# Performance work log

Measured on AMD Instinct MI355X. Metric: run time of the kernel, lower is better.

Reference implementation:

```python
import jax, jax.numpy as jnp
import numpy as np

L, B, T, C, H, D, F, W = 2, 2, 2048, 1024, 16, 64, 4096, 256
NEG = -1e9
EPS = 1e-6


def _rms(x, g):
    return x * jax.lax.rsqrt(jnp.mean(x * x, axis=-1, keepdims=True) + EPS) * g


def setup_inputs() -> dict:
    key = jax.random.key(0)
    ks = jax.random.split(key, 12)
    s = 0.02
    return {
        "x": jax.random.normal(ks[0], (B, T, C), jnp.float32),
        "retrieval_context": jax.random.normal(ks[1], (B, C), jnp.float32),
        "norm1_g": jnp.ones((L, C), jnp.float32),
        "Wqkv": jax.random.normal(ks[2], (L, C, 3 * C), jnp.float32) * s,
        "Wproj": jax.random.normal(ks[3], (L, C, C), jnp.float32) * s,
        "gate_W": jax.random.normal(ks[4], (L, C, 3), jnp.float32) * 0.01,
        "gate_b": jnp.zeros((L, 3), jnp.float32),
        "ret_W": jax.random.normal(ks[5], (L, C, C), jnp.float32) * 0.01,
        "norm2_g": jnp.ones((L, C), jnp.float32),
        "ffn_gate_W": jax.random.normal(ks[6], (L, C, F), jnp.float32) * s,
        "ffn_up_W": jax.random.normal(ks[7], (L, C, F), jnp.float32) * s,
        "ffn_down_W": jax.random.normal(ks[8], (L, F, C), jnp.float32) * s,
    }


def reference(x, retrieval_context, norm1_g, Wqkv, Wproj, gate_W, gate_b, ret_W,
              norm2_g, ffn_gate_W, ffn_up_W, ffn_down_W):
    # Sliding-window causal mask: key j visible to query i iff i-W+1 <= j <= i
    pos = jnp.arange(T)
    allowed = (pos[None, :] <= pos[:, None]) & (pos[None, :] >= pos[:, None] - W + 1)
    mask = jnp.where(allowed, 0.0, NEG).astype(x.dtype)  # (T, T)
    scale = 1.0 / np.sqrt(D)

    for l in range(L):
        h = _rms(x, norm1_g[l])                              # (B,T,C)
        qkv = h @ Wqkv[l]                                    # (B,T,3C)
        q, k, v = jnp.split(qkv, 3, axis=-1)
        q = q.reshape(B, T, H, D).transpose(0, 2, 1, 3)       # (B,H,T,D)
        k = k.reshape(B, T, H, D).transpose(0, 2, 1, 3)
        v = v.reshape(B, T, H, D).transpose(0, 2, 1, 3)
        scores = jnp.einsum("bhqd,bhkd->bhqk", q, k) * scale + mask
        attn = jax.nn.softmax(scores, axis=-1)
        o = jnp.einsum("bhqk,bhkd->bhqd", attn, v)
        attn_out = o.transpose(0, 2, 1, 3).reshape(B, T, C) @ Wproj[l]

        # TRN disabled: trn_out == 0, gate channel 1 pinned to -1e9
        gate_logits = h @ gate_W[l] + gate_b[l]               # (B,T,3)
        gate_logits = gate_logits.at[..., 1].set(NEG)
        gates = jax.nn.softmax(gate_logits, axis=-1)

        ret_out = (retrieval_context @ ret_W[l])[:, None, :]   # (B,1,C) broadcast over T
        mixed = gates[..., 0:1] * attn_out + gates[..., 2:3] * ret_out
        x = x + mixed

        h2 = _rms(x, norm2_g[l])
        ffn = (jax.nn.silu(h2 @ ffn_gate_W[l]) * (h2 @ ffn_up_W[l])) @ ffn_down_W[l]
        x = x + ffn
    return x
```

## Files before the change

kernel.cpp:

```cpp
#include <hip/hip_runtime.h>

#define L_ 2
#define B_ 2
#define T_ 2048
#define C_ 1024
#define H_ 16
#define D_ 64
#define F_ 4096
#define NTOK 4096
#define NELEM 4194304

typedef unsigned short u16;
typedef __attribute__((ext_vector_type(8))) short short8;
typedef __attribute__((ext_vector_type(4))) float float4v;

__device__ __forceinline__ float bf2f(u16 u) {
  unsigned v = ((unsigned)u) << 16;
  return __builtin_bit_cast(float, v);
}
__device__ __forceinline__ u16 f2bf(float f) {
  unsigned u = __builtin_bit_cast(unsigned, f);
  u += 0x7FFFu + ((u >> 16) & 1u);
  return (u16)(u >> 16);
}

__global__ void k_copyf(const float* __restrict__ in, float* __restrict__ out) {
  const int i = blockIdx.x * 256 + threadIdx.x;
  out[i] = in[i];
}

__device__ __forceinline__ void rms_tail(float* vloc, const float* __restrict__ g,
                                         u16* __restrict__ orow) {
  float s = vloc[0] * vloc[0] + vloc[1] * vloc[1] + vloc[2] * vloc[2] + vloc[3] * vloc[3];
#pragma unroll
  for (int o = 32; o; o >>= 1) s += __shfl_down(s, o);
  __shared__ float red[4];
  __shared__ float rsv;
  if ((threadIdx.x & 63) == 0) red[threadIdx.x >> 6] = s;
  __syncthreads();
  if (threadIdx.x == 0) {
    float t = red[0] + red[1] + red[2] + red[3];
    rsv = rsqrtf(t * (1.f / C_) + 1e-6f);
  }
  __syncthreads();
  const float rr = rsv;
#pragma unroll
  for (int i = 0; i < 4; i++) {
    const int c = threadIdx.x + i * 256;
    orow[c] = f2bf(vloc[i] * rr * g[c]);
  }
}

__global__ __launch_bounds__(256) void k_rms_first(const float* __restrict__ xin,
                                                   const float* __restrict__ g,
                                                   float* __restrict__ x,
                                                   u16* __restrict__ out) {
  const int row = blockIdx.x;
  const float* sr = xin + (size_t)row * C_;
  float* xr = x + (size_t)row * C_;
  float vloc[4];
#pragma unroll
  for (int i = 0; i < 4; i++) {
    const int c = threadIdx.x + i * 256;
    const float v = sr[c];
    vloc[i] = v;
    xr[c] = v;
  }
  rms_tail(vloc, g, out + (size_t)row * C_);
}

__global__ __launch_bounds__(256) void k_rms(const float* __restrict__ x,
                                             const float* __restrict__ g,
                                             u16* __restrict__ out) {
  const int row = blockIdx.x;
  const float* xr = x + (size_t)row * C_;
  float vloc[4];
#pragma unroll
  for (int i = 0; i < 4; i++) vloc[i] = xr[threadIdx.x + i * 256];
  rms_tail(vloc, g, out + (size_t)row * C_);
}

__global__ __launch_bounds__(256) void k_rms2mix(float* __restrict__ x,
                                                 const float* __restrict__ gates,
                                                 const float* __restrict__ ret,
                                                 const float* __restrict__ g,
                                                 u16* __restrict__ out) {
  const int row = blockIdx.x;
  const int b = row >> 11;
  const float g2 = gates[row * 2 + 1];
  const float* rr_ = ret + b * C_;
  float* xr = x + (size_t)row * C_;
  float vloc[4];
#pragma unroll
  for (int i = 0; i < 4; i++) {
    const int c = threadIdx.x + i * 256;
    const float v = xr[c] + g2 * rr_[c];
    vloc[i] = v;
    xr[c] = v;
  }
  rms_tail(vloc, g, out + (size_t)row * C_);
}

__global__ void k_tr2(const float* __restrict__ s0, u16* __restrict__ d0,
                      int K0, int N0, int t0,
                      const float* __restrict__ s1, u16* __restrict__ d1,
                      int K1, int N1) {
  __shared__ float tile[32][33];
  int t = blockIdx.x;
  const float* src; u16* dst; int K, N;
  if (t < t0) { src = s0; dst = d0; K = K0; N = N0; }
  else { t -= t0; src = s1; dst = d1; K = K1; N = N1; }
  const int ntx = N >> 5;
  const int tx = t % ntx, ty = t / ntx;
  const int x = tx * 32 + threadIdx.x;
  const int y0 = ty * 32 + threadIdx.y;
#pragma unroll
  for (int i = 0; i < 32; i += 8) tile[threadIdx.y + i][threadIdx.x] = src[(size_t)(y0 + i) * N + x];
  __syncthreads();
  const int x2 = ty * 32 + threadIdx.x;
  const int y2 = tx * 32 + threadIdx.y;
#pragma unroll
  for (int i = 0; i < 32; i += 8) dst[(size_t)(y2 + i) * K + x2] = f2bf(tile[threadIdx.x][threadIdx.y + i]);
}

__global__ void k_tr1(const float* __restrict__ in, u16* __restrict__ out, int K, int N) {
  __shared__ float tile[32][33];
  const int ntx = N >> 5;
  const int tx = blockIdx.x % ntx, ty = blockIdx.x / ntx;
  const int x = tx * 32 + threadIdx.x;
  const int y0 = ty * 32 + threadIdx.y;
#pragma unroll
  for (int i = 0; i < 32; i += 8) tile[threadIdx.y + i][threadIdx.x] = in[(size_t)(y0 + i) * N + x];
  __syncthreads();
  const int x2 = ty * 32 + threadIdx.x;
  const int y2 = tx * 32 + threadIdx.y;
#pragma unroll
  for (int i = 0; i < 32; i += 8) out[(size_t)(y2 + i) * K + x2] = f2bf(tile[threadIdx.x][threadIdx.y + i]);
}

__global__ void k_vt(const u16* __restrict__ qkv, u16* __restrict__ Vt) {
  __shared__ u16 tile[32][34];
  const int jt = blockIdx.x;
  const int dt = blockIdx.y;
  const int bh = blockIdx.z;
  const int b = bh >> 4;
  const int h = bh & 15;
  const int tx = threadIdx.x, ty = threadIdx.y;
#pragma unroll
  for (int i = 0; i < 32; i += 8) {
    const int j = jt * 32 + ty + i;
    const int d = dt * 32 + tx;
    tile[ty + i][tx] = qkv[(size_t)(b * T_ + j) * (3 * C_) + 2 * C_ + h * D_ + d];
  }
  __syncthreads();
#pragma unroll
  for (int i = 0; i < 32; i += 8) {
    const int d = dt * 32 + ty + i;
    const int j = jt * 32 + tx;
    Vt[(size_t)(bh * D_ + d) * T_ + j] = tile[tx][ty + i];
  }
}

template <int EPI>
__global__ __launch_bounds__(256) void k_gemm_bt(const u16* __restrict__ A,
                                                 const u16* __restrict__ Bt,
                                                 u16* __restrict__ Cc,
                                                 float* __restrict__ Xf,
                                                 const float* __restrict__ gates,
                                                 int N, int K) {
  __shared__ __align__(16) u16 As[128 * 64];
  __shared__ __align__(16) u16 Bs[128 * 64];
  const int tid = threadIdx.x;
  const int wave = tid >> 6;
  const int lane = tid & 63;
  const int quad = lane >> 4;
  const int m16 = lane & 15;
  const int m0 = blockIdx.x * 128;
  const int n0 = blockIdx.y * 128;
  const int wm = (wave & 1) * 64;
  const int wn = (wave >> 1) * 64;
  const int srow = lane >> 3;
  const int sc = lane & 7;
  const int scol = ((sc ^ srow) & 7) * 8;
  const int csw = m16 & 7;
  const int Kslice = K / gridDim.z;
  const int kbeg = blockIdx.z * Kslice;

  float4v acc[4][4];
#pragma unroll
  for (int i = 0; i < 4; i++)
#pragma unroll
    for (int j = 0; j < 4; j++) acc[i][j] = (float4v){0.f, 0.f, 0.f, 0.f};

  for (int k0 = kbeg; k0 < kbeg + Kslice; k0 += 64) {
#pragma unroll
    for (int p = 0; p < 4; p++) {
      const int r = p * 32 + wave * 8;
      const u16* ga = A + (size_t)(m0 + r + srow) * K + k0 + scol;
      const u16* gb = Bt + (size_t)(n0 + r + srow) * K + k0 + scol;
      __builtin_amdgcn_global_load_lds((const __attribute__((address_space(1))) void*)ga,
                                       (__attribute__((address_space(3))) void*)((char*)As + r * 128),
                                       16, 0, 0);
      __builtin_amdgcn_global_load_lds((const __attribute__((address_space(1))) void*)gb,
                                       (__attribute__((address_space(3))) void*)((char*)Bs + r * 128),
                                       16, 0, 0);
    }
    __syncthreads();
#pragma unroll
    for (int s = 0; s < 2; s++) {
      const int chunk = ((s * 4 + quad) ^ csw) * 16;
      short8 af[4], bfr[4];
#pragma unroll
      for (int i = 0; i < 4; i++) {
        af[i] = *(const short8*)((const char*)As + (wm + i * 16 + m16) * 128 + chunk);
        bfr[i] = *(const short8*)((const char*)Bs + (wn + i * 16 + m16) * 128 + chunk);
      }
#pragma unroll
      for (int i = 0; i < 4; i++)
#pragma unroll
        for (int j = 0; j < 4; j++)
          acc[i][j] = __builtin_amdgcn_mfma_f32_16x16x32_bf16(af[i], bfr[j], acc[i][j], 0, 0, 0);
    }
    __syncthreads();
  }
#pragma unroll
  for (int i = 0; i < 4; i++) {
    const int row0 = m0 + wm + i * 16 + quad * 4;
#pragma unroll
    for (int j = 0; j < 4; j++) {
      const int col = n0 + wn + j * 16 + m16;
#pragma unroll
      for (int r = 0; r < 4; r++) {
        const size_t idx = (size_t)(row0 + r) * N + col;
        const float v = acc[i][j][r];
        if (EPI == 0) Cc[idx] = f2bf(v);
        else if (EPI == 1) unsafeAtomicAdd(&Xf[idx], gates[(row0 + r) * 2] * v);
        else unsafeAtomicAdd(&Xf[idx], v);
      }
    }
  }
}

__global__ __launch_bounds__(256) void k_gemm_swiglu(const u16* __restrict__ A,
                                                     const u16* __restrict__ Btg,
                                                     const u16* __restrict__ Btu,
                                                     u16* __restrict__ Cc,
                                                     int N, int K) {
  __shared__ __align__(16) u16 As[128 * 64];
  __shared__ __align__(16) u16 Bsg[128 * 64];
  __shared__ __align__(16) u16 Bsu[128 * 64];
  const int tid = threadIdx.x;
  const int wave = tid >> 6;
  const int lane = tid & 63;
  const int quad = lane >> 4;
  const int m16 = lane & 15;
  const int m0 = blockIdx.x * 128;
  const int n0 = blockIdx.y * 128;
  const int wm = (wave & 1) * 64;
  const int wn = (wave >> 1) * 64;
  const int srow = lane >> 3;
  const int sc = lane & 7;
  const int scol = ((sc ^ srow) & 7) * 8;
  const int csw = m16 & 7;

  float4v accg[4][4], accu[4][4];
#pragma unroll
  for (int i = 0; i < 4; i++)
#pragma unroll
    for (int j = 0; j < 4; j++) {
      accg[i][j] = (float4v){0.f, 0.f, 0.f, 0.f};
      accu[i][j] = (float4v){0.f, 0.f, 0.f, 0.f};
    }

  for (int k0 = 0; k0 < K; k0 += 64) {
#pragma unroll
    for (int p = 0; p < 4; p++) {
      const int r = p * 32 + wave * 8;
      const u16* ga = A + (size_t)(m0 + r + srow) * K + k0 + scol;
      const u16* gg = Btg + (size_t)(n0 + r + srow) * K + k0 + scol;
      const u16* gu = Btu + (size_t)(n0 + r + srow) * K + k0 + scol;
      __builtin_amdgcn_global_load_lds((const __attribute__((address_space(1))) void*)ga,
                                       (__attribute__((address_space(3))) void*)((char*)As + r * 128),
                                       16, 0, 0);
      __builtin_amdgcn_global_load_lds((const __attribute__((address_space(1))) void*)gg,
                                       (__attribute__((address_space(3))) void*)((char*)Bsg + r * 128),
                                       16, 0, 0);
      __builtin_amdgcn_global_load_lds((const __attribute__((address_space(1))) void*)gu,
                                       (__attribute__((address_space(3))) void*)((char*)Bsu + r * 128),
                                       16, 0, 0);
    }
    __syncthreads();
#pragma unroll
    for (int s = 0; s < 2; s++) {
      const int chunk = ((s * 4 + quad) ^ csw) * 16;
      short8 af[4], bg[4], bu[4];
#pragma unroll
      for (int i = 0; i < 4; i++) {
        af[i] = *(const short8*)((const char*)As + (wm + i * 16 + m16) * 128 + chunk);
        bg[i] = *(const short8*)((const char*)Bsg + (wn + i * 16 + m16) * 128 + chunk);
        bu[i] = *(const short8*)((const char*)Bsu + (wn + i * 16 + m16) * 128 + chunk);
      }
#pragma unroll
      for (int i = 0; i < 4; i++)
#pragma unroll
        for (int j = 0; j < 4; j++) {
          accg[i][j] = __builtin_amdgcn_mfma_f32_16x16x32_bf16(af[i], bg[j], accg[i][j], 0, 0, 0);
          accu[i][j] = __builtin_amdgcn_mfma_f32_16x16x32_bf16(af[i], bu[j], accu[i][j], 0, 0, 0);
        }
    }
    __syncthreads();
  }
#pragma unroll
  for (int i = 0; i < 4; i++) {
    const int row0 = m0 + wm + i * 16 + quad * 4;
#pragma unroll
    for (int j = 0; j < 4; j++) {
      const int col = n0 + wn + j * 16 + m16;
#pragma unroll
      for (int r = 0; r < 4; r++) {
        const float g = accg[i][j][r];
        const float u = accu[i][j][r];
        Cc[(size_t)(row0 + r) * N + col] = f2bf(u * g / (1.f + __expf(-g)));
      }
    }
  }
}

__global__ __launch_bounds__(256) void k_attn(const u16* __restrict__ qkv,
                                              const u16* __restrict__ Vt,
                                              u16* __restrict__ o) {
  __shared__ u16 lds[4][16][290];
  const int wave = threadIdx.x >> 6;
  const int widG = blockIdx.x * 4 + wave;
  const int lane = threadIdx.x & 63;
  const int quad = lane >> 4;
  const int c16 = lane & 15;
  const int qt = (widG & 127) * 16;
  const int h = (widG >> 7) & 15;
  const int b = widG >> 11;
  const size_t rs = 3 * C_;
  const int jt0 = qt - 256;

  const u16* qrow = qkv + (size_t)(b * T_ + qt + c16) * rs + h * D_ + quad * 8;
  const short8 a0 = *(const short8*)(qrow);
  const short8 a1 = *(const short8*)(qrow + 32);
  float4v S[17];
  const short8 z8 = (short8){0, 0, 0, 0, 0, 0, 0, 0};
#pragma unroll
  for (int t = 0; t < 17; t++) {
    if (jt0 + t * 16 + 15 < 0) { S[t] = (float4v){0.f, 0.f, 0.f, 0.f}; continue; }
    const int j = jt0 + t * 16 + c16;
    short8 b0 = z8, b1 = z8;
    if (j >= 0) {
      const u16* krow = qkv + (size_t)(b * T_ + j) * rs + C_ + h * D_ + quad * 8;
      b0 = *(const short8*)(krow);
      b1 = *(const short8*)(krow + 32);
    }
    float4v z = (float4v){0.f, 0.f, 0.f, 0.f};
    z = __builtin_amdgcn_mfma_f32_16x16x32_bf16(a0, b0, z, 0, 0, 0);
    z = __builtin_amdgcn_mfma_f32_16x16x32_bf16(a1, b1, z, 0, 0, 0);
    S[t] = z;
  }
#pragma unroll
  for (int r = 0; r < 4; r++) {
    const int q = qt + quad * 4 + r;
    float mx = -1.0e30f;
#pragma unroll
    for (int t = 0; t < 17; t++) {
      const int j = jt0 + t * 16 + c16;
      const int w = j - q + 255;
      const bool vis = (j >= 0) && (w >= 0) && (w < 256);
      if (vis) {
        const float s = S[t][r] * 0.125f;
        S[t][r] = s;
        mx = fmaxf(mx, s);
      } else {
        S[t][r] = -1.0e30f;
      }
    }
#pragma unroll
    for (int o2 = 1; o2 < 16; o2 <<= 1) mx = fmaxf(mx, __shfl_xor(mx, o2));
    float sum = 0.f;
#pragma unroll
    for (int t = 0; t < 17; t++) {
      const float e = (S[t][r] > -0.9e30f) ? __expf(S[t][r] - mx) : 0.f;
      S[t][r] = e;
      sum += e;
    }
#pragma unroll
    for (int o2 = 1; o2 < 16; o2 <<= 1) sum += __shfl_xor(sum, o2);
    const float inv = 1.f / fmaxf(sum, 1e-30f);
    const int prow = quad * 4 + r;
#pragma unroll
    for (int t = 0; t < 17; t++) lds[wave][prow][t * 16 + c16] = f2bf(S[t][r] * inv);
    lds[wave][prow][272 + c16] = 0;
  }
  __syncthreads();

  float4v acc[4];
#pragma unroll
  for (int md = 0; md < 4; md++) acc[md] = (float4v){0.f, 0.f, 0.f, 0.f};
  const u16* vtb = Vt + (size_t)((b * H_ + h) * D_) * T_;
  const uint* prow32 = (const uint*)(&lds[wave][c16][0]);
  union { short8 s8; uint u[4]; } bf;
#pragma unroll
  for (int c = 0; c < 9; c++) {
    const int jbase = jt0 + c * 32;
    if (jbase + 31 < 0) continue;
#pragma unroll
    for (int w2 = 0; w2 < 4; w2++) bf.u[w2] = prow32[c * 16 + quad * 4 + w2];
    int j0 = jbase + quad * 8;
    j0 = (j0 < 0) ? 0 : ((j0 > T_ - 8) ? (T_ - 8) : j0);
#pragma unroll
    for (int md = 0; md < 4; md++) {
      const short8 af = *(const short8*)(vtb + (size_t)(md * 16 + c16) * T_ + j0);
      acc[md] = __builtin_amdgcn_mfma_f32_16x16x32_bf16(af, bf.s8, acc[md], 0, 0, 0);
    }
  }
#pragma unroll
  for (int md = 0; md < 4; md++) {
    uint u0 = (uint)f2bf(acc[md][0]) | ((uint)f2bf(acc[md][1]) << 16);
    uint u1 = (uint)f2bf(acc[md][2]) | ((uint)f2bf(acc[md][3]) << 16);
    uint2 pk = make_uint2(u0, u1);
    u16* dst = o + (size_t)(b * T_ + qt + c16) * C_ + h * D_ + md * 16 + quad * 4;
    *(uint2*)dst = pk;
  }
}

__global__ __launch_bounds__(256) void k_gate(const u16* __restrict__ h,
                                              const float* __restrict__ gW,
                                              const float* __restrict__ gb,
                                              float* __restrict__ gates) {
  const int row = blockIdx.x * 4 + (threadIdx.x >> 6);
  const int lane = threadIdx.x & 63;
  const u16* hr = h + (size_t)row * C_;
  float s0 = 0.f, s2 = 0.f;
  for (int k = lane; k < C_; k += 64) {
    const float hv = bf2f(hr[k]);
    s0 += hv * gW[k * 3 + 0];
    s2 += hv * gW[k * 3 + 2];
  }
#pragma unroll
  for (int o = 32; o; o >>= 1) { s0 += __shfl_down(s0, o); s2 += __shfl_down(s2, o); }
  if (lane == 0) {
    const float l0 = s0 + gb[0];
    const float l2 = s2 + gb[2];
    const float m = fmaxf(l0, l2);
    const float e0 = __expf(l0 - m), e2 = __expf(l2 - m);
    const float inv = 1.f / (e0 + e2);
    gates[row * 2 + 0] = e0 * inv;
    gates[row * 2 + 1] = e2 * inv;
  }
}

__global__ void k_ret2(const float* __restrict__ rc, const float* __restrict__ rW,
                       float* __restrict__ ret) {
  const int l = blockIdx.x >> 3;
  const int bid = blockIdx.x & 7;
  const int b = bid >> 2;
  const int col = (bid & 3) * 256 + threadIdx.x;
  const float* rWl = rW + (size_t)l * C_ * C_;
  float s = 0.f;
  for (int k = 0; k < C_; k++) s += rc[b * C_ + k] * rWl[(size_t)k * C_ + col];
  ret[(size_t)l * B_ * C_ + b * C_ + col] = s;
}

extern "C" void kernel_launch(void* const* d_in, const int* in_sizes, int n_in,
                              void* d_out, int out_size, void* d_ws, size_t ws_size,
                              hipStream_t stream) {
  (void)in_sizes; (void)n_in; (void)out_size; (void)ws_size;
  const float* xin  = (const float*)d_in[0];
  const float* rc   = (const float*)d_in[1];
  const float* n1g  = (const float*)d_in[2];
  const float* Wqkv = (const float*)d_in[3];
  const float* Wpro = (const float*)d_in[4];
  const float* gW   = (const float*)d_in[5];
  const float* gb   = (const float*)d_in[6];
  const float* rW   = (const float*)d_in[7];
  const float* n2g  = (const float*)d_in[8];
  const float* fgW  = (const float*)d_in[9];
  const float* fuW  = (const float*)d_in[10];
  const float* fdW  = (const float*)d_in[11];

  char* w = (char*)d_ws;
  float* gates = (float*)(w);
  float* retb  = (float*)(w + 32768);
  float* xf32  = (float*)(w + 65536);
  u16* hbuf    = (u16*)(w + 65536 + (size_t)NELEM * 4);
  u16* big     = hbuf + NELEM;
  u16* qkv  = big;
  u16* obuf = big + (size_t)NTOK * 3 * C_;
  u16* gbuf = big;
  u16* wT  = (u16*)d_out;
  u16* wTp = wT + (size_t)3 * C_ * C_;
  u16* Vt  = (u16*)d_out + (size_t)NELEM;
  u16* wT2 = Vt;

  k_ret2<<<16, 256, 0, stream>>>(rc, rW, retb);

  for (int l = 0; l < L_; l++) {
    if (l == 0)
      k_rms_first<<<NTOK, 256, 0, stream>>>(xin, n1g, xf32, hbuf);
    else
      k_rms<<<NTOK, 256, 0, stream>>>(xf32, n1g + l * C_, hbuf);
    k_tr2<<<3072 + 1024, dim3(32, 8), 0, stream>>>(
        Wqkv + (size_t)l * C_ * 3 * C_, wT, C_, 3 * C_, 3072,
        Wpro + (size_t)l * C_ * C_, wTp, C_, C_);
    k_gemm_bt<0><<<dim3(NTOK / 128, 3 * C_ / 128, 1), 256, 0, stream>>>(
        hbuf, wT, qkv, nullptr, nullptr, 3 * C_, C_);
    k_gate<<<NTOK / 4, 256, 0, stream>>>(hbuf, gW + (size_t)l * C_ * 3, gb + l * 3, gates);
    k_vt<<<dim3(64, 2, 32), dim3(32, 8), 0, stream>>>(qkv, Vt);
    k_attn<<<1024, 256, 0, stream>>>(qkv, Vt, obuf);
    k_gemm_bt<1><<<dim3(NTOK / 128, C_ / 128, 2), 256, 0, stream>>>(
        obuf, wTp, nullptr, xf32, gates, C_, C_);
    k_rms2mix<<<NTOK, 256, 0, stream>>>(xf32, gates, retb + (size_t)l * B_ * C_,
                                        n2g + l * C_, hbuf);
    k_tr2<<<4096 + 4096, dim3(32, 8), 0, stream>>>(
        fgW + (size_t)l * C_ * F_, wT, C_, F_, 4096,
        fuW + (size_t)l * C_ * F_, wT2, C_, F_);
    k_gemm_swiglu<<<dim3(NTOK / 128, F_ / 128), 256, 0, stream>>>(
        hbuf, wT, wT2, gbuf, F_, C_);
    k_tr1<<<4096, dim3(32, 8), 0, stream>>>(fdW + (size_t)l * F_ * C_, hbuf, F_, C_);
    k_gemm_bt<2><<<dim3(NTOK / 128, C_ / 128, 2), 256, 0, stream>>>(
        gbuf, hbuf, nullptr, xf32, nullptr, C_, F_);
  }

  k_copyf<<<NELEM / 256, 256, 0, stream>>>(xf32, (float*)d_out);
}
```

Before: 913.8 us.

## Replace GEMMs with 256x256 double-buffered 8-wave ping-pong MFMA kernels

Replaces the 128x128 single-buffered GEMM and SwiGLU kernels with 512-thread, 256-tile kernels that use 128KB of dynamic LDS. Global-to-LDS loads are double-buffered and interleaved with MFMA phases, using explicit barriers, waitcnt and s_setprio to overlap memory with compute. The aim is more reuse per block and hidden load latency. The cost is large register and LDS footprint, fewer blocks in the grid, and fragile hand-placed waitcnt and barrier ordering.

Measured after the change: 843.6 us. -7.7%, faster.

```diff
diff --git a/kernel.cpp b/kernel.cpp
--- a/kernel.cpp
+++ b/kernel.cpp
@@ -161,74 +161,154 @@
   }
 }
 
+
+#define VMW(n) asm volatile("s_waitcnt vmcnt(" #n ")" ::: "memory")
+#define LGKM0 asm volatile("s_waitcnt lgkmcnt(0)" ::: "memory")
+#define GBAR() __builtin_amdgcn_s_barrier()
+#define PRIO1() __builtin_amdgcn_s_setprio(1)
+#define PRIO0() __builtin_amdgcn_s_setprio(0)
+
+#define STG8(gsrc, grow0, dstbyte, kk)                                                    \
+  do {                                                                                    \
+    const u16* g0_ = (gsrc) + (size_t)((grow0) + wid * 8 + srow) * K + (kk) + scol;       \
+    __builtin_amdgcn_global_load_lds(                                                     \
+        (const __attribute__((address_space(1))) void*)g0_,                               \
+        (__attribute__((address_space(3))) void*)(lc + (dstbyte) + wid * 8 * 128),        \
+        16, 0, 0);                                                                        \
+    const u16* g1_ = g0_ + (size_t)64 * K;                                                \
+    __builtin_amdgcn_global_load_lds(                                                     \
+        (const __attribute__((address_space(1))) void*)g1_,                               \
+        (__attribute__((address_space(3))) void*)(lc + (dstbyte) + (64 + wid * 8) * 128), \
+        16, 0, 0);                                                                        \
+  } while (0)
+
+#define RDA4(dst, bufbyte, ig0)                                                           \
+  { _Pragma("unroll") for (int i_ = 0; i_ < 4; ++i_) {                                    \
+      _Pragma("unroll") for (int s_ = 0; s_ < 2; ++s_)                                    \
+        dst[i_][s_] = *(const short8*)(lc + (bufbyte) +                                   \
+            (wm * 128 + ((ig0) + i_) * 16 + m16) * 128 + (((s_ * 4 + quad) ^ csw) * 16)); } }
+
+#define RDB4(dst, bufbyte, jg0)                                                           \
+  { _Pragma("unroll") for (int j_ = 0; j_ < 2; ++j_) {                                    \
+      _Pragma("unroll") for (int s_ = 0; s_ < 2; ++s_)                                    \
+        dst[j_][s_] = *(const short8*)(lc + (bufbyte) +                                   \
+            (wn * 64 + ((jg0) + j_) * 16 + m16) * 128 + (((s_ * 4 + quad) ^ csw) * 16)); } }
+
+#define RDBS(dst, bufbyte)                                                                \
+  { _Pragma("unroll") for (int j_ = 0; j_ < 2; ++j_) {                                    \
+      _Pragma("unroll") for (int s_ = 0; s_ < 2; ++s_)                                    \
+        dst[j_][s_] = *(const short8*)(lc + (bufbyte) +                                   \
+            (wn * 32 + j_ * 16 + m16) * 128 + (((s_ * 4 + quad) ^ csw) * 16)); } }
+
+#define MM16(ig0, jg0, bv_)                                                               \
+  { _Pragma("unroll") for (int i_ = 0; i_ < 4; ++i_) {                                    \
+      _Pragma("unroll") for (int j_ = 0; j_ < 2; ++j_) {                                  \
+        _Pragma("unroll") for (int s_ = 0; s_ < 2; ++s_)                                  \
+          acc[(ig0) + i_][(jg0) + j_] = __builtin_amdgcn_mfma_f32_16x16x32_bf16(          \
+              av[i_][s_], bv_[j_][s_], acc[(ig0) + i_][(jg0) + j_], 0, 0, 0); } } }
+
+#define MMS(accv, ig0, bv_)                                                               \
+  { _Pragma("unroll") for (int i_ = 0; i_ < 4; ++i_) {                                    \
+      _Pragma("unroll") for (int j_ = 0; j_ < 2; ++j_) {                                  \
+        _Pragma("unroll") for (int s_ = 0; s_ < 2; ++s_)                                  \
+          accv[(ig0) + i_][j_] = __builtin_amdgcn_mfma_f32_16x16x32_bf16(                 \
+              av[i_][s_], bv_[j_][s_], accv[(ig0) + i_][j_], 0, 0, 0); } } }
+
 template <int EPI>
-__global__ __launch_bounds__(256) void k_gemm_bt(const u16* __restrict__ A,
+__global__ __launch_bounds__(512, 2) void k_g256(const u16* __restrict__ A,
                                                  const u16* __restrict__ Bt,
                                                  u16* __restrict__ Cc,
                                                  float* __restrict__ Xf,
                                                  const float* __restrict__ gates,
                                                  int N, int K) {
-  __shared__ __align__(16) u16 As[128 * 64];
-  __shared__ __align__(16) u16 Bs[128 * 64];
+  extern __shared__ __align__(16) u16 lds[];
+  char* const lc = (char*)lds;
+  enum { A0B = 0, B0B = 32768, A1B = 65536, B1B = 98304 };
   const int tid = threadIdx.x;
-  const int wave = tid >> 6;
-  const int lane = tid & 63;
-  const int quad = lane >> 4;
-  const int m16 = lane & 15;
-  const int m0 = blockIdx.x * 128;
-  const int n0 = blockIdx.y * 128;
-  const int wm = (wave & 1) * 64;
-  const int wn = (wave >> 1) * 64;
-  const int srow = lane >> 3;
-  const int sc = lane & 7;
+  const int wid = tid >> 6, lane = tid & 63;
+  const int wm = wid >> 2, wn = wid & 3;
+  const int quad = lane >> 4, m16 = lane & 15;
+  const int srow = lane >> 3, sc = lane & 7;
   const int scol = ((sc ^ srow) & 7) * 8;
   const int csw = m16 & 7;
+  const int m0 = blockIdx.x * 256, n0 = blockIdx.y * 256;
   const int Kslice = K / gridDim.z;
   const int kbeg = blockIdx.z * Kslice;
-
-  float4v acc[4][4];
-#pragma unroll
-  for (int i = 0; i < 4; i++)
+  const int ntile = Kslice >> 6;
+  const int nit = ntile >> 1;
+
+  float4v acc[8][4];
+#pragma unroll
+  for (int i = 0; i < 8; i++)
 #pragma unroll
     for (int j = 0; j < 4; j++) acc[i][j] = (float4v){0.f, 0.f, 0.f, 0.f};
-
-  for (int k0 = kbeg; k0 < kbeg + Kslice; k0 += 64) {
-#pragma unroll
-    for (int p = 0; p < 4; p++) {
-      const int r = p * 32 + wave * 8;
-      const u16* ga = A + (size_t)(m0 + r + srow) * K + k0 + scol;
-      const u16* gb = Bt + (size_t)(n0 + r + srow) * K + k0 + scol;
-      __builtin_amdgcn_global_load_lds((const __attribute__((address_space(1))) void*)ga,
-                                       (__attribute__((address_space(3))) void*)((char*)As + r * 128),
-                                       16, 0, 0);
-      __builtin_amdgcn_global_load_lds((const __attribute__((address_space(1))) void*)gb,
-                                       (__attribute__((address_space(3))) void*)((char*)Bs + r * 128),
-                                       16, 0, 0);
-    }
-    __syncthreads();
-#pragma unroll
-    for (int s = 0; s < 2; s++) {
-      const int chunk = ((s * 4 + quad) ^ csw) * 16;
-      short8 af[4], bfr[4];
-#pragma unroll
-      for (int i = 0; i < 4; i++) {
-        af[i] = *(const short8*)((const char*)As + (wm + i * 16 + m16) * 128 + chunk);
-        bfr[i] = *(const short8*)((const char*)Bs + (wn + i * 16 + m16) * 128 + chunk);
-      }
-#pragma unroll
-      for (int i = 0; i < 4; i++)
-#pragma unroll
-        for (int j = 0; j < 4; j++)
-          acc[i][j] = __builtin_amdgcn_mfma_f32_16x16x32_bf16(af[i], bfr[j], acc[i][j], 0, 0, 0);
-    }
-    __syncthreads();
-  }
-#pragma unroll
-  for (int i = 0; i < 4; i++) {
-    const int row0 = m0 + wm + i * 16 + quad * 4;
+  short8 av[4][2], b01[2][2], b23[2][2];
+
+  STG8(Bt, n0, B0B, kbeg);
+  STG8(Bt, n0 + 128, B0B + 16384, kbeg);
+  STG8(A, m0, A0B, kbeg);
+  STG8(A, m0 + 128, A0B + 16384, kbeg);
+  STG8(Bt, n0, B1B, kbeg + 64);
+  STG8(Bt, n0 + 128, B1B + 16384, kbeg + 64);
+  VMW(4);
+  GBAR();
+
+#pragma unroll 1
+  for (int it = 0; it < nit; ++it) {
+    const int t2 = 2 * it + 2, t3 = 2 * it + 3;
+    const int k1 = kbeg + (2 * it + 1) * 64;
+    const int k2 = kbeg + (t2 < ntile ? t2 : t2 - ntile) * 64;
+    const int k3 = kbeg + (t3 < ntile ? t3 : t3 - ntile) * 64;
+    RDA4(av, A0B, 0);
+    RDB4(b01, B0B, 0);
+    STG8(A, m0, A1B, k1);
+    GBAR(); LGKM0;
+    PRIO1(); MM16(0, 0, b01); PRIO0();
+    GBAR();
+    RDB4(b23, B0B, 2);
+    STG8(A, m0 + 128, A1B + 16384, k1);
+    GBAR(); LGKM0;
+    PRIO1(); MM16(0, 2, b23); PRIO0();
+    GBAR();
+    RDA4(av, A0B, 4);
+    STG8(Bt, n0, B0B, k2);
+    GBAR(); LGKM0;
+    PRIO1(); MM16(4, 2, b23); PRIO0();
+    GBAR();
+    STG8(Bt, n0 + 128, B0B + 16384, k2);
+    VMW(4);
+    GBAR(); LGKM0;
+    PRIO1(); MM16(4, 0, b01); PRIO0();
+    GBAR();
+    RDA4(av, A1B, 0);
+    RDB4(b01, B1B, 0);
+    STG8(A, m0, A0B, k2);
+    GBAR(); LGKM0;
+    PRIO1(); MM16(0, 0, b01); PRIO0();
+    GBAR();
+    RDB4(b23, B1B, 2);
+    STG8(A, m0 + 128, A0B + 16384, k2);
+    GBAR(); LGKM0;
+    PRIO1(); MM16(0, 2, b23); PRIO0();
+    GBAR();
+    RDA4(av, A1B, 4);
+    STG8(Bt, n0, B1B, k3);
+    GBAR(); LGKM0;
+    PRIO1(); MM16(4, 2, b23); PRIO0();
+    GBAR();
+    STG8(Bt, n0 + 128, B1B + 16384, k3);
+    VMW(4);
+    GBAR(); LGKM0;
+    PRIO1(); MM16(4, 0, b01); PRIO0();
+    GBAR();
+  }
+
+#pragma unroll
+  for (int i = 0; i < 8; i++) {
+    const int row0 = m0 + wm * 128 + i * 16 + quad * 4;
 #pragma unroll
     for (int j = 0; j < 4; j++) {
-      const int col = n0 + wn + j * 16 + m16;
+      const int col = n0 + wn * 64 + j * 16 + m16;
 #pragma unroll
       for (int r = 0; r < 4; r++) {
         const size_t idx = (size_t)(row0 + r) * N + col;
@@ -241,81 +321,102 @@
   }
 }
 
-__global__ __launch_bounds__(256) void k_gemm_swiglu(const u16* __restrict__ A,
-                                                     const u16* __restrict__ Btg,
-                                                     const u16* __restrict__ Btu,
-                                                     u16* __restrict__ Cc,
-                                                     int N, int K) {
-  __shared__ __align__(16) u16 As[128 * 64];
-  __shared__ __align__(16) u16 Bsg[128 * 64];
-  __shared__ __align__(16) u16 Bsu[128 * 64];
+__global__ __launch_bounds__(512, 2) void k_g256s(const u16* __restrict__ A,
+                                                  const u16* __restrict__ Btg,
+                                                  const u16* __restrict__ Btu,
+                                                  u16* __restrict__ Cc,
+                                                  int N, int K) {
+  extern __shared__ __align__(16) u16 lds[];
+  char* const lc = (char*)lds;
+  enum { SA0 = 0, SG0 = 32768, SU0 = 49152, SA1 = 65536, SG1 = 98304, SU1 = 114688 };
   const int tid = threadIdx.x;
-  const int wave = tid >> 6;
-  const int lane = tid & 63;
-  const int quad = lane >> 4;
-  const int m16 = lane & 15;
-  const int m0 = blockIdx.x * 128;
-  const int n0 = blockIdx.y * 128;
-  const int wm = (wave & 1) * 64;
-  const int wn = (wave >> 1) * 64;
-  const int srow = lane >> 3;
-  const int sc = lane & 7;
+  const int wid = tid >> 6, lane = tid & 63;
+  const int wm = wid >> 2, wn = wid & 3;
+  const int quad = lane >> 4, m16 = lane & 15;
+  const int srow = lane >> 3, sc = lane & 7;
   const int scol = ((sc ^ srow) & 7) * 8;
   const int csw = m16 & 7;
-
-  float4v accg[4][4], accu[4][4];
-#pragma unroll
-  for (int i = 0; i < 4; i++)
-#pragma unroll
-    for (int j = 0; j < 4; j++) {
+  const int m0 = blockIdx.x * 256, n0 = blockIdx.y * 128;
+  const int kbeg = 0;
+  const int ntile = K >> 6;
+  const int nit = ntile >> 1;
+
+  float4v accg[8][2], accu[8][2];
+#pragma unroll
+  for (int i = 0; i < 8; i++)
+#pragma unroll
+    for (int j = 0; j < 2; j++) {
       accg[i][j] = (float4v){0.f, 0.f, 0.f, 0.f};
       accu[i][j] = (float4v){0.f, 0.f, 0.f, 0.f};
     }
-
-  for (int k0 = 0; k0 < K; k0 += 64) {
-#pragma unroll
-    for (int p = 0; p < 4; p++) {
-      const int r = p * 32 + wave * 8;
-      const u16* ga = A + (size_t)(m0 + r + srow) * K + k0 + scol;
-      const u16* gg = Btg + (size_t)(n0 + r + srow) * K + k0 + scol;
-      const u16* gu = Btu + (size_t)(n0 + r + srow) * K + k0 + scol;
-      __builtin_amdgcn_global_load_lds((const __attribute__((address_space(1))) void*)ga,
-                                       (__attribute__((address_space(3))) void*)((char*)As + r * 128),
-                                       16, 0, 0);
-      __builtin_amdgcn_global_load_lds((const __attribute__((address_space(1))) void*)gg,
-                                       (__attribute__((address_space(3))) void*)((char*)Bsg + r * 128),
-                                       16, 0, 0);
-      __builtin_amdgcn_global_load_lds((const __attribute__((address_space(1))) void*)gu,
-                                       (__attribute__((address_space(3))) void*)((char*)Bsu + r * 128),
-                                       16, 0, 0);
-    }
-    __syncthreads();
-#pragma unroll
-    for (int s = 0; s < 2; s++) {
-      const int chunk = ((s * 4 + quad) ^ csw) * 16;
-      short8 af[4], bg[4], bu[4];
-#pragma unroll
-      for (int i = 0; i < 4; i++) {
-        af[i] = *(const short8*)((const char*)As + (wm + i * 16 + m16) * 128 + chunk);
-        bg[i] = *(const short8*)((const char*)Bsg + (wn + i * 16 + m16) * 128 + chunk);
-        bu[i] = *(const short8*)((const char*)Bsu + (wn + i * 16 + m16) * 128 + chunk);
-      }
-#pragma unroll
-      for (int i = 0; i < 4; i++)
-#pragma unroll
-        for (int j = 0; j < 4; j++) {
-          accg[i][j] = __builtin_amdgcn_mfma_f32_16x16x32_bf16(af[i], bg[j], accg[i][j], 0, 0, 0);
-          accu[i][j] = __builtin_amdgcn_mfma_f32_16x16x32_bf16(af[i], bu[j], accu[i][j], 0, 0, 0);
-        }
-    }
-    __syncthreads();
-  }
-#pragma unroll
-  for (int i = 0; i < 4; i++) {
-    const int row0 = m0 + wm + i * 16 + quad * 4;
-#pragma unroll
-    for (int j = 0; j < 4; j++) {
-      const int col = n0 + wn + j * 16 + m16;
+  short8 av[4][2], bg[2][2], bu[2][2];
+
+  STG8(Btg, n0, SG0, kbeg);
+  STG8(Btu, n0, SU0, kbeg);
+  STG8(A, m0, SA0, kbeg);
+  STG8(A, m0 + 128, SA0 + 16384, kbeg);
+  STG8(Btg, n0, SG1, kbeg + 64);
+  STG8(Btu, n0, SU1, kbeg + 64);
+  STG8(A, m0, SA1, kbeg + 64);
+  VMW(6);
+  GBAR();
+
+#pragma unroll 1
+  for (int it = 0; it < nit; ++it) {
+    const int t2 = 2 * it + 2, t3 = 2 * it + 3;
+    const int k1 = kbeg + (2 * it + 1) * 64;
+    const int k2 = kbeg + (t2 < ntile ? t2 : t2 - ntile) * 64;
+    const int k3 = kbeg + (t3 < ntile ? t3 : t3 - ntile) * 64;
+    RDA4(av, SA0, 0);
+    RDBS(bg, SG0);
+    STG8(A, m0 + 128, SA1 + 16384, k1);
+    GBAR(); LGKM0;
+    PRIO1(); MMS(accg, 0, bg); PRIO0();
+    GBAR();
+    RDBS(bu, SU0);
+    STG8(Btg, n0, SG0, k2);
+    GBAR(); LGKM0;
+    PRIO1(); MMS(accu, 0, bu); PRIO0();
+    GBAR();
+    RDA4(av, SA0, 4);
+    STG8(Btu, n0, SU0, k2);
+    GBAR(); LGKM0;
+    PRIO1(); MMS(accu, 4, bu); PRIO0();
+    GBAR();
+    STG8(A, m0, SA0, k2);
+    VMW(6);
+    GBAR(); LGKM0;
+    PRIO1(); MMS(accg, 4, bg); PRIO0();
+    GBAR();
+    RDA4(av, SA1, 0);
+    RDBS(bg, SG1);
+    STG8(A, m0 + 128, SA0 + 16384, k2);
+    GBAR(); LGKM0;
+    PRIO1(); MMS(accg, 0, bg); PRIO0();
+    GBAR();
+    RDBS(bu, SU1);
+    STG8(Btg, n0, SG1, k3);
+    GBAR(); LGKM0;
+    PRIO1(); MMS(accu, 0, bu); PRIO0();
+    GBAR();
+    RDA4(av, SA1, 4);
+    STG8(Btu, n0, SU1, k3);
+    GBAR(); LGKM0;
+    PRIO1(); MMS(accu, 4, bu); PRIO0();
+    GBAR();
+    STG8(A, m0, SA1, k3);
+    VMW(6);
+    GBAR(); LGKM0;
+    PRIO1(); MMS(accg, 4, bg); PRIO0();
+    GBAR();
+  }
+
+#pragma unroll
+  for (int i = 0; i < 8; i++) {
+    const int row0 = m0 + wm * 128 + i * 16 + quad * 4;
+#pragma unroll
+    for (int j = 0; j < 2; j++) {
+      const int col = n0 + wn * 32 + j * 16 + m16;
 #pragma unroll
       for (int r = 0; r < 4; r++) {
         const float g = accg[i][j][r];
@@ -482,6 +583,15 @@
   const float* fuW  = (const float*)d_in[10];
   const float* fdW  = (const float*)d_in[11];
 
+  static bool attr_done = false;
+  if (!attr_done) {
+    hipFuncSetAttribute((const void*)k_g256<0>, hipFuncAttributeMaxDynamicSharedMemorySize, 131072);
+    hipFuncSetAttribute((const void*)k_g256<1>, hipFuncAttributeMaxDynamicSharedMemorySize, 131072);
+    hipFuncSetAttribute((const void*)k_g256<2>, hipFuncAttributeMaxDynamicSharedMemorySize, 131072);
+    hipFuncSetAttribute((const void*)k_g256s, hipFuncAttributeMaxDynamicSharedMemorySize, 131072);
+    attr_done = true;
+  }
+
   char* w = (char*)d_ws;
   float* gates = (float*)(w);
   float* retb  = (float*)(w + 32768);
@@ -506,22 +616,22 @@
     k_tr2<<<3072 + 1024, dim3(32, 8), 0, stream>>>(
         Wqkv + (size_t)l * C_ * 3 * C_, wT, C_, 3 * C_, 3072,
         Wpro + (size_t)l * C_ * C_, wTp, C_, C_);
-    k_gemm_bt<0><<<dim3(NTOK / 128, 3 * C_ / 128, 1), 256, 0, stream>>>(
+    k_g256<0><<<dim3(NTOK / 256, 3 * C_ / 256, 1), 512, 131072, stream>>>(
         hbuf, wT, qkv, nullptr, nullptr, 3 * C_, C_);
     k_gate<<<NTOK / 4, 256, 0, stream>>>(hbuf, gW + (size_t)l * C_ * 3, gb + l * 3, gates);
     k_vt<<<dim3(64, 2, 32), dim3(32, 8), 0, stream>>>(qkv, Vt);
     k_attn<<<1024, 256, 0, stream>>>(qkv, Vt, obuf);
-    k_gemm_bt<1><<<dim3(NTOK / 128, C_ / 128, 2), 256, 0, stream>>>(
+    k_g256<1><<<dim3(NTOK / 256, C_ / 256, 2), 512, 131072, stream>>>(
         obuf, wTp, nullptr, xf32, gates, C_, C_);
     k_rms2mix<<<NTOK, 256, 0, stream>>>(xf32, gates, retb + (size_t)l * B_ * C_,
                                         n2g + l * C_, hbuf);
     k_tr2<<<4096 + 4096, dim3(32, 8), 0, stream>>>(
         fgW + (size_t)l * C_ * F_, wT, C_, F_, 4096,
         fuW + (size_t)l * C_ * F_, wT2, C_, F_);
-    k_gemm_swiglu<<<dim3(NTOK / 128, F_ / 128), 256, 0, stream>>>(
+    k_g256s<<<dim3(NTOK / 256, F_ / 128, 1), 512, 131072, stream>>>(
         hbuf, wT, wT2, gbuf, F_, C_);
     k_tr1<<<4096, dim3(32, 8), 0, stream>>>(fdW + (size_t)l * F_ * C_, hbuf, F_, C_);
-    k_gemm_bt<2><<<dim3(NTOK / 128, C_ / 128, 2), 256, 0, stream>>>(
+    k_g256<2><<<dim3(NTOK / 256, C_ / 256, 4), 512, 131072, stream>>>(
         gbuf, hbuf, nullptr, xf32, nullptr, C_, F_);
   }
 
```
